# Performance work log

Hardware: AMD Instinct MI355X
Metric: run time of the kernel (lower is better)

Reference implementation:

```python
import jax, jax.numpy as jnp
import numpy as np

C_IN = 64      # in_channels
C_OUT = 64     # out_channels
LOC = 2        # locality_size
K = 2 * LOC + 1   # kernel size = 5
B, H, W = 4, 128, 128


def _init_lateral_weights():
    # Matches LateralLayer._init_lateral_weights: 1 at (co, co*K*K + LOC*K + LOC)
    w = np.zeros((C_OUT, C_IN * K * K), np.float32)
    for co in range(C_OUT):
        cii = co * K * K + LOC * K + LOC  # center tap of matching input channel
        w[co, cii] = 1.0
    return jnp.asarray(w).reshape(C_OUT, C_IN * K * K, 1, 1)


def setup_inputs() -> dict:
    key = jax.random.key(0)
    # binary input (the layer asserts x in {0,1})
    x = jax.random.bernoulli(key, 0.1, (B, C_IN, H, W)).astype(jnp.float32)
    return {"x": x, "W_lateral": _init_lateral_weights()}


def _rearrange(x):
    # Faithful to F.conv2d(x, W_rearrange, padding='same') with the one-hot
    # indicator kernel: out[b, i*K*K + j*K + kk, h, w] = x_pad[b, i, h+j, w+kk].
    # Implemented as an unfold via K*K shifted slices (same math, no O((CKK)^2) conv).
    p = LOC
    xp = jnp.pad(x, ((0, 0), (0, 0), (p, p), (p, p)))
    Hh, Ww = x.shape[2], x.shape[3]
    patches = [xp[:, :, j:j + Hh, kk:kk + Ww] for j in range(K) for kk in range(K)]
    xr = jnp.stack(patches, axis=2)              # (B, C, K*K, H, W)
    return xr.reshape(x.shape[0], x.shape[1] * K * K, Hh, Ww)


def reference(x, W_lateral):
    xr = _rearrange(x)                                  # (B, C*K*K, H, W)
    w = W_lateral.reshape(W_lateral.shape[0], -1)       # (O, C*K*K)
    # 1x1 conv == channel contraction
    x_lateral = jnp.einsum('bkhw,ok->bohw', xr, w)      # (B, O, H, W)
    # conv with ones_like(W_lateral) == channel sum, same for every out channel
    x_max_act = jnp.sum(xr, axis=1, keepdims=True)      # (B, 1, H, W)
    min_support = float(K)
    x_max_act = jnp.maximum(x_max_act, min_support)
    xn = x_lateral / x_max_act
    xn = xn / (1e-10 + jnp.sum(w, axis=1)[None, :, None, None])
    xn = xn / (1e-10 + jnp.max(xn, axis=(2, 3), keepdims=True))
    # ts == 0 -> no temporal averaging with x_lateral_norm_prev
    x_lateral_bin = (xn ** 3 >= 0.5).astype(jnp.float32)
    return x_lateral, xn, x_lateral_bin
```

## Files before the change

### kernel.cpp

```cpp
#include <hip/hip_runtime.h>

constexpr int Bb  = 4;
constexpr int C   = 64;
constexpr int H   = 128;
constexpr int Wd  = 128;
constexpr int K   = 5;
constexpr int LOC = 2;
constexpr int KK  = K * K;
constexpr int CKK = C * KK;
constexpr int HW  = H * Wd;
constexpr int N   = Bb * C * HW;
constexpr int BHW = Bb * HW;

__device__ __forceinline__ float frcp(float x) { return __builtin_amdgcn_rcpf(x); }

__global__ void k_chansum(const float* __restrict__ x, float* __restrict__ S) {
    int i = blockIdx.x * 256 + threadIdx.x;
    int b = i >> 14;
    int p = i & (HW - 1);
    const float* px = x + (size_t)b * C * HW + p;
    float s = 0.0f;
#pragma unroll
    for (int c = 0; c < C; ++c) s += px[c * HW];
    S[i] = s;
}

__global__ void k_box(const float* __restrict__ S, float* __restrict__ M) {
    int i = blockIdx.x * 256 + threadIdx.x;
    int b = i >> 14;
    int p = i & (HW - 1);
    int h = p >> 7, w = p & 127;
    const float* Sb = S + b * HW;
    float s = 0.0f;
#pragma unroll
    for (int j = 0; j < K; ++j) {
        int hh = h + j - LOC;
        if ((unsigned)hh >= (unsigned)H) continue;
        const float* row = Sb + hh * Wd;
#pragma unroll
        for (int kk = 0; kk < K; ++kk) {
            int ww = w + kk - LOC;
            if ((unsigned)ww < (unsigned)Wd) s += row[ww];
        }
    }
    M[i] = fmaxf(s, (float)K);
}

__global__ void __launch_bounds__(512, 1) k_main(
    const float* __restrict__ x, const float* __restrict__ wgt,
    const float* __restrict__ M, float* __restrict__ out0,
    float* __restrict__ out1, float* __restrict__ out2) {
    __shared__ int   s_k[CKK];
    __shared__ float s_v[CKK];
    __shared__ int   s_cnt;
    __shared__ float s_wsum;
    __shared__ float s_red[8];
    __shared__ float s_rinv;

    const int tid = threadIdx.x;
    const int plane = blockIdx.x;
    const int o = plane & (C - 1);
    const int b = plane >> 6;

    if (tid == 0) { s_cnt = 0; s_wsum = 0.0f; }
    __syncthreads();

    const float* wrow = wgt + o * CKK;
    for (int k = tid; k < CKK; k += 512) {
        float v = wrow[k];
        if (v != 0.0f) {
            int pos = atomicAdd(&s_cnt, 1);
            s_k[pos] = k;
            s_v[pos] = v;
            atomicAdd(&s_wsum, v);
        }
    }
    __syncthreads();
    const int   n   = s_cnt;
    const float rws = frcp(1e-10f + s_wsum);

    const float* xb = x + (size_t)b * C * HW;
    float* o0 = out0 + (size_t)plane * HW;
    float* o1 = out1 + (size_t)plane * HW;
    float* o2 = out2 + (size_t)plane * HW;
    const float* Mb = M + b * HW;

    float4 t[8];
    float lmax = -INFINITY;
#pragma unroll
    for (int it = 0; it < 8; ++it) {
        const int p = it * 2048 + tid * 4;
        const int h = p >> 7, w = p & 127;
        float4 acc = {0.f, 0.f, 0.f, 0.f};
        for (int e = 0; e < n; ++e) {
            const int   k = s_k[e];
            const float v = s_v[e];
            const int c  = k / KK;
            const int r  = k - c * KK;
            const int rj = r / K;
            const int dj = rj - LOC;
            const int dk = (r - rj * K) - LOC;
            const int hh = h + dj;
            if ((unsigned)hh < (unsigned)H) {
                const float* rowp = xb + c * HW + hh * Wd;
                const int wb = w + dk;
                float x0 = ((unsigned)(wb + 0) < (unsigned)Wd) ? rowp[wb + 0] : 0.f;
                float x1 = ((unsigned)(wb + 1) < (unsigned)Wd) ? rowp[wb + 1] : 0.f;
                float x2 = ((unsigned)(wb + 2) < (unsigned)Wd) ? rowp[wb + 2] : 0.f;
                float x3 = ((unsigned)(wb + 3) < (unsigned)Wd) ? rowp[wb + 3] : 0.f;
                acc.x += v * x0; acc.y += v * x1; acc.z += v * x2; acc.w += v * x3;
            }
        }
        *reinterpret_cast<float4*>(o0 + p) = acc;
        const float4 Mv = *reinterpret_cast<const float4*>(Mb + p);
        float4 tv;
        tv.x = acc.x * frcp(Mv.x) * rws;
        tv.y = acc.y * frcp(Mv.y) * rws;
        tv.z = acc.z * frcp(Mv.z) * rws;
        tv.w = acc.w * frcp(Mv.w) * rws;
        t[it] = tv;
        lmax = fmaxf(lmax, fmaxf(fmaxf(tv.x, tv.y), fmaxf(tv.z, tv.w)));
    }

#pragma unroll
    for (int m = 32; m > 0; m >>= 1) lmax = fmaxf(lmax, __shfl_xor(lmax, m, 64));
    if ((tid & 63) == 0) s_red[tid >> 6] = lmax;
    __syncthreads();
    if (tid == 0) {
        float r = s_red[0];
#pragma unroll
        for (int q = 1; q < 8; ++q) r = fmaxf(r, s_red[q]);
        s_rinv = frcp(1e-10f + r);
    }
    __syncthreads();
    const float rinv = s_rinv;

#pragma unroll
    for (int it = 0; it < 8; ++it) {
        const int p = it * 2048 + tid * 4;
        const float4 tv = t[it];
        float4 xn, bn;
        xn.x = tv.x * rinv; xn.y = tv.y * rinv; xn.z = tv.z * rinv; xn.w = tv.w * rinv;
        bn.x = (xn.x * xn.x * xn.x >= 0.5f) ? 1.f : 0.f;
        bn.y = (xn.y * xn.y * xn.y >= 0.5f) ? 1.f : 0.f;
        bn.z = (xn.z * xn.z * xn.z >= 0.5f) ? 1.f : 0.f;
        bn.w = (xn.w * xn.w * xn.w >= 0.5f) ? 1.f : 0.f;
        *reinterpret_cast<float4*>(o1 + p) = xn;
        *reinterpret_cast<float4*>(o2 + p) = bn;
    }
}

extern "C" void kernel_launch(void* const* d_in, const int* in_sizes, int n_in,
                              void* d_out, int out_size, void* d_ws, size_t ws_size,
                              hipStream_t stream) {
    const float* x   = (const float*)d_in[0];
    const float* wgt = (const float*)d_in[1];
    float* out = (float*)d_out;
    float* wsf = (float*)d_ws;

    float* S = wsf;
    float* M = wsf + BHW;

    float* out0 = out;
    float* out1 = out + N;
    float* out2 = out + 2 * N;

    k_chansum<<<BHW / 256, 256, 0, stream>>>(x, S);
    k_box<<<BHW / 256, 256, 0, stream>>>(S, M);
    k_main<<<Bb * C, 512, 0, stream>>>(x, wgt, M, out0, out1, out2);
}
```

Baseline: 103.8 us.

## Fuse channel-sum and box filter into one prep kernel; widen main blocks, nontemporal stores

Merges the channel-sum and 5x5 box-filter kernels into a single kernel that sums channels for a 6-row halo strip into shared memory, then applies the box filter from LDS. This removes one launch and the global round trip of the intermediate sum buffer. The halo rows get recomputed, so each strip reads 3x the rows it outputs. The main kernel now runs 1024 threads per block with 4 iterations each, and all outputs use nontemporal stores to avoid polluting the cache.

```diff
diff --git a/kernel.cpp b/kernel.cpp
--- a/kernel.cpp
+++ b/kernel.cpp
@@ -10,43 +10,56 @@
 constexpr int CKK = C * KK;
 constexpr int HW  = H * Wd;
 constexpr int N   = Bb * C * HW;
-constexpr int BHW = Bb * HW;
+
+typedef float v4f __attribute__((ext_vector_type(4)));
 
 __device__ __forceinline__ float frcp(float x) { return __builtin_amdgcn_rcpf(x); }
-
-__global__ void k_chansum(const float* __restrict__ x, float* __restrict__ S) {
-    int i = blockIdx.x * 256 + threadIdx.x;
-    int b = i >> 14;
-    int p = i & (HW - 1);
-    const float* px = x + (size_t)b * C * HW + p;
-    float s = 0.0f;
-#pragma unroll
-    for (int c = 0; c < C; ++c) s += px[c * HW];
-    S[i] = s;
+__device__ __forceinline__ void nt_store4(float* p, v4f v) {
+    __builtin_nontemporal_store(v, reinterpret_cast<v4f*>(p));
 }
 
-__global__ void k_box(const float* __restrict__ S, float* __restrict__ M) {
-    int i = blockIdx.x * 256 + threadIdx.x;
-    int b = i >> 14;
-    int p = i & (HW - 1);
-    int h = p >> 7, w = p & 127;
-    const float* Sb = S + b * HW;
-    float s = 0.0f;
+__global__ void __launch_bounds__(256) k_prep(const float* __restrict__ x,
+                                              float* __restrict__ M) {
+    __shared__ float S[6][Wd];
+    const int t = threadIdx.x;
+    const int b = blockIdx.x >> 6;
+    const int strip = blockIdx.x & 63;
+    const int r0 = strip * 2;
+
+    if (t < 192) {
+        const int lr = t >> 5;
+        const int c0 = (t & 31) * 4;
+        const int gr = r0 - 2 + lr;
+        v4f s = {0.f, 0.f, 0.f, 0.f};
+        if ((unsigned)gr < (unsigned)H) {
+            const float* p = x + (((size_t)b * C) * H + gr) * Wd + c0;
+#pragma unroll
+            for (int c = 0; c < C; ++c) {
+                const v4f v = *reinterpret_cast<const v4f*>(p + (size_t)c * HW);
+                s += v;
+            }
+        }
+        *reinterpret_cast<v4f*>(&S[lr][c0]) = s;
+    }
+    __syncthreads();
+
+    const int lr = t >> 7;
+    const int w  = t & 127;
+    const int gr = r0 + lr;
+    float s = 0.f;
 #pragma unroll
     for (int j = 0; j < K; ++j) {
-        int hh = h + j - LOC;
-        if ((unsigned)hh >= (unsigned)H) continue;
-        const float* row = Sb + hh * Wd;
+        const float* row = S[lr + j];
 #pragma unroll
         for (int kk = 0; kk < K; ++kk) {
-            int ww = w + kk - LOC;
+            const int ww = w + kk - LOC;
             if ((unsigned)ww < (unsigned)Wd) s += row[ww];
         }
     }
-    M[i] = fmaxf(s, (float)K);
+    M[b * HW + gr * Wd + w] = fmaxf(s, (float)K);
 }
 
-__global__ void __launch_bounds__(512, 1) k_main(
+__global__ void __launch_bounds__(1024) k_main(
     const float* __restrict__ x, const float* __restrict__ wgt,
     const float* __restrict__ M, float* __restrict__ out0,
     float* __restrict__ out1, float* __restrict__ out2) {
@@ -54,7 +67,7 @@
     __shared__ float s_v[CKK];
     __shared__ int   s_cnt;
     __shared__ float s_wsum;
-    __shared__ float s_red[8];
+    __shared__ float s_red[16];
     __shared__ float s_rinv;
 
     const int tid = threadIdx.x;
@@ -66,7 +79,7 @@
     __syncthreads();
 
     const float* wrow = wgt + o * CKK;
-    for (int k = tid; k < CKK; k += 512) {
+    for (int k = tid; k < CKK; k += 1024) {
         float v = wrow[k];
         if (v != 0.0f) {
             int pos = atomicAdd(&s_cnt, 1);
@@ -85,13 +98,13 @@
     float* o2 = out2 + (size_t)plane * HW;
     const float* Mb = M + b * HW;
 
-    float4 t[8];
+    v4f t[4];
     float lmax = -INFINITY;
 #pragma unroll
-    for (int it = 0; it < 8; ++it) {
-        const int p = it * 2048 + tid * 4;
+    for (int it = 0; it < 4; ++it) {
+        const int p = it * 4096 + tid * 4;
         const int h = p >> 7, w = p & 127;
-        float4 acc = {0.f, 0.f, 0.f, 0.f};
+        v4f acc = {0.f, 0.f, 0.f, 0.f};
         for (int e = 0; e < n; ++e) {
             const int   k = s_k[e];
             const float v = s_v[e];
@@ -111,9 +124,9 @@
                 acc.x += v * x0; acc.y += v * x1; acc.z += v * x2; acc.w += v * x3;
             }
         }
-        *reinterpret_cast<float4*>(o0 + p) = acc;
-        const float4 Mv = *reinterpret_cast<const float4*>(Mb + p);
-        float4 tv;
+        nt_store4(o0 + p, acc);
+        const v4f Mv = *reinterpret_cast<const v4f*>(Mb + p);
+        v4f tv;
         tv.x = acc.x * frcp(Mv.x) * rws;
         tv.y = acc.y * frcp(Mv.y) * rws;
         tv.z = acc.z * frcp(Mv.z) * rws;
@@ -129,24 +142,24 @@
     if (tid == 0) {
         float r = s_red[0];
 #pragma unroll
-        for (int q = 1; q < 8; ++q) r = fmaxf(r, s_red[q]);
+        for (int q = 1; q < 16; ++q) r = fmaxf(r, s_red[q]);
         s_rinv = frcp(1e-10f + r);
     }
     __syncthreads();
     const float rinv = s_rinv;
 
 #pragma unroll
-    for (int it = 0; it < 8; ++it) {
-        const int p = it * 2048 + tid * 4;
-        const float4 tv = t[it];
-        float4 xn, bn;
-        xn.x = tv.x * rinv; xn.y = tv.y * rinv; xn.z = tv.z * rinv; xn.w = tv.w * rinv;
+    for (int it = 0; it < 4; ++it) {
+        const int p = it * 4096 + tid * 4;
+        const v4f tv = t[it];
+        v4f xn, bn;
+        xn = tv * rinv;
         bn.x = (xn.x * xn.x * xn.x >= 0.5f) ? 1.f : 0.f;
         bn.y = (xn.y * xn.y * xn.y >= 0.5f) ? 1.f : 0.f;
         bn.z = (xn.z * xn.z * xn.z >= 0.5f) ? 1.f : 0.f;
         bn.w = (xn.w * xn.w * xn.w >= 0.5f) ? 1.f : 0.f;
-        *reinterpret_cast<float4*>(o1 + p) = xn;
-        *reinterpret_cast<float4*>(o2 + p) = bn;
+        nt_store4(o1 + p, xn);
+        nt_store4(o2 + p, bn);
     }
 }
 
@@ -156,16 +169,12 @@
     const float* x   = (const float*)d_in[0];
     const float* wgt = (const float*)d_in[1];
     float* out = (float*)d_out;
-    float* wsf = (float*)d_ws;
-
-    float* S = wsf;
-    float* M = wsf + BHW;
+    float* M   = (float*)d_ws;
 
     float* out0 = out;
     float* out1 = out + N;
     float* out2 = out + 2 * N;
 
-    k_chansum<<<BHW / 256, 256, 0, stream>>>(x, S);
-    k_box<<<BHW / 256, 256, 0, stream>>>(S, M);
-    k_main<<<Bb * C, 512, 0, stream>>>(x, wgt, M, out0, out1, out2);
+    k_prep<<<Bb * 64, 256, 0, stream>>>(x, M);
+    k_main<<<Bb * C, 1024, 0, stream>>>(x, wgt, M, out0, out1, out2);
 }
```

Measured after the change: 92.46 us. -10.9%, faster.
